# Kernel optimization log

Hardware: AMD Instinct MI355X
Metric: run time of the kernel (lower is better)

## Reference

```python
import jax, jax.numpy as jnp
import numpy as np

DIM, WIDTH = 5, 64
BATCH, N_SAVE = 4096, 64
RTOL, ATOL = 1e-3, 1e-6
SAFETY, FMIN, FMAX = 0.9, 0.2, 10.0
MAX_STEPS, DT0, EPS = 64, 0.1, 1e-6

# Tsit5 (Tsitouras 2011) Butcher tableau
A21 = 0.161
A31, A32 = -0.008480655492356989, 0.335480655492357
A41, A42, A43 = 2.8971530571054935, -6.359448489975075, 4.3622954328695815
A51, A52, A53, A54 = 5.325864828439257, -11.748883564062828, 7.4955393428898365, -0.09249506636175525
A61, A62, A63, A64, A65 = 5.86145544294642, -12.92096931784711, 8.159367898576159, -0.071584973281401, -0.028269050394068383
B1, B2, B3, B4, B5, B6 = 0.09646076681806523, 0.01, 0.4798896504144996, 1.379008574103742, -3.290069515436081, 2.324710524099774
# embedded 4th-order error coefficients (b - bhat)
E1, E2, E3, E4, E5, E6, E7 = (-0.00178001105222577714, -0.0008164344596567469,
    0.007880878010261995, -0.1447110071732629, 0.5823571654525552,
    -0.45808210592918697, 0.015151515151515152)


def _mlp(y, W1, b1, W2, b2, W3, b3, W4, b4):
    # eqx.nn.MLP(5, 5, width 64, depth 3, softplus)
    h = jax.nn.softplus(y @ W1.T + b1)
    h = jax.nn.softplus(h @ W2.T + b2)
    h = jax.nn.softplus(h @ W3.T + b3)
    return h @ W4.T + b4


def _solve_one(y0, t_eval, params):
    f = lambda y: _mlp(y, *params)
    t0, t1 = t_eval[0], t_eval[-1]
    # save points at/before t0 get y0
    ys0 = jnp.where((t_eval <= t0 + EPS)[:, None], y0[None, :], 0.0)

    def body(carry, _):
        t, y, h, ys = carry
        done = t >= t1 - EPS
        hc = jnp.where(done, 0.0, jnp.minimum(h, t1 - t))  # clip last step to t1
        k1 = f(y)
        k2 = f(y + hc * (A21 * k1))
        k3 = f(y + hc * (A31 * k1 + A32 * k2))
        k4 = f(y + hc * (A41 * k1 + A42 * k2 + A43 * k3))
        k5 = f(y + hc * (A51 * k1 + A52 * k2 + A53 * k3 + A54 * k4))
        k6 = f(y + hc * (A61 * k1 + A62 * k2 + A63 * k3 + A64 * k4 + A65 * k5))
        ynew = y + hc * (B1 * k1 + B2 * k2 + B3 * k3 + B4 * k4 + B5 * k5 + B6 * k6)
        k7 = f(ynew)  # FSAL stage, also used for error + interpolation
        err = hc * (E1 * k1 + E2 * k2 + E3 * k3 + E4 * k4 + E5 * k5 + E6 * k6 + E7 * k7)
        scale = ATOL + RTOL * jnp.maximum(jnp.abs(y), jnp.abs(ynew))
        enorm = jnp.sqrt(jnp.mean((err / scale) ** 2))
        enorm_c = jax.lax.stop_gradient(jnp.maximum(enorm, 1e-10))
        accept = enorm <= 1.0
        factor = jnp.clip(SAFETY * enorm_c ** -0.2, FMIN, FMAX)  # I-controller, order 5
        step_ok = accept & ~done
        t_next = jnp.where(step_ok, t + hc, t)
        y_next = jnp.where(step_ok, ynew, y)
        h_next = jnp.where(done, h, hc * factor)
        # cubic Hermite interpolation for save points inside (t, t_next]
        s = ((t_eval - t) / jnp.maximum(hc, 1e-12))[:, None]
        h00 = 2 * s**3 - 3 * s**2 + 1
        h10 = s**3 - 2 * s**2 + s
        h01 = -2 * s**3 + 3 * s**2
        h11 = s**3 - s**2
        yi = h00 * y + h10 * hc * k1 + h01 * ynew + h11 * hc * k7
        mask = (t_eval > t) & (t_eval <= t_next + EPS) & step_ok
        ys = jnp.where(mask[:, None], yi, ys)
        return (t_next, y_next, h_next, ys), None

    h0 = jnp.asarray(DT0, dtype=y0.dtype)
    (_, _, _, ys), _ = jax.lax.scan(body, (t0, y0, h0, ys0), None, length=MAX_STEPS)
    return ys  # [N_SAVE, DIM]


def setup_inputs() -> dict:
    key = jax.random.key(0)
    ks = jax.random.split(key, 9)
    y0 = jax.random.normal(ks[0], (BATCH, DIM), dtype=jnp.float32)
    t_eval = jnp.linspace(0.0, 1.0, N_SAVE, dtype=jnp.float32)

    def lin(k, out_d, in_d):
        lim = 1.0 / np.sqrt(in_d)
        kw, kb = jax.random.split(k)
        W = jax.random.uniform(kw, (out_d, in_d), jnp.float32, -lim, lim)
        b = jax.random.uniform(kb, (out_d,), jnp.float32, -lim, lim)
        return W, b

    W1, b1 = lin(ks[1], WIDTH, DIM)
    W2, b2 = lin(ks[2], WIDTH, WIDTH)
    W3, b3 = lin(ks[3], WIDTH, WIDTH)
    W4, b4 = lin(ks[4], DIM, WIDTH)
    return {"y0": y0, "t_eval": t_eval, "W1": W1, "b1": b1, "W2": W2, "b2": b2,
            "W3": W3, "b3": b3, "W4": W4, "b4": b4}


def reference(y0, t_eval, W1, b1, W2, b2, W3, b3, W4, b4):
    params = (W1, b1, W2, b2, W3, b3, W4, b4)
    return jax.vmap(lambda y: _solve_one(y, t_eval, params))(y0)  # [BATCH, N_SAVE, DIM]
```

## Files before the change

kernel.cpp:

```cpp
#include <hip/hip_runtime.h>
#include <cmath>

namespace {

constexpr int kDim = 5;
constexpr int kSave = 64;
constexpr int kTraj = 16;
constexpr int kThreads = 256;
constexpr int kMaxSteps = 64;
constexpr int HS = 72;
constexpr int SD = 8;

typedef _Float16 half8 __attribute__((ext_vector_type(8)));
typedef float f32x4 __attribute__((ext_vector_type(4)));

__device__ __forceinline__ float softplusf(float x) {
  return fmaxf(x, 0.0f) + __logf(1.0f + __expf(-fabsf(x)));
}

__global__ __launch_bounds__(kThreads, 1)
void node_tsit5_kernel(const float* __restrict__ gy0,
                       const float* __restrict__ gte,
                       const float* __restrict__ gW1, const float* __restrict__ gb1,
                       const float* __restrict__ gW2, const float* __restrict__ gb2,
                       const float* __restrict__ gW3, const float* __restrict__ gb3,
                       const float* __restrict__ gW4, const float* __restrict__ gb4,
                       float* __restrict__ out) {
  const float A21 = 0.161f;
  const float A31 = -0.008480655492356989f, A32 = 0.335480655492357f;
  const float A41 = 2.8971530571054935f, A42 = -6.359448489975075f, A43 = 4.3622954328695815f;
  const float A51 = 5.325864828439257f, A52 = -11.748883564062828f, A53 = 7.4955393428898365f,
              A54 = -0.09249506636175525f;
  const float A61 = 5.86145544294642f, A62 = -12.92096931784711f, A63 = 8.159367898576159f,
              A64 = -0.071584973281401f, A65 = -0.028269050394068383f;
  const float B1 = 0.09646076681806523f, B2 = 0.01f, B3 = 0.4798896504144996f,
              B4 = 1.379008574103742f, B5 = -3.290069515436081f, B6 = 2.324710524099774f;
  const float E1 = -0.00178001105222577714f, E2 = -0.0008164344596567469f,
              E3 = 0.007880878010261995f, E4 = -0.1447110071732629f, E5 = 0.5823571654525552f,
              E6 = -0.45808210592918697f, E7 = 0.015151515151515152f;

  __shared__ __align__(16) _Float16 h0[kTraj * HS], l0[kTraj * HS];
  __shared__ __align__(16) _Float16 h1[kTraj * HS], l1[kTraj * HS];
  __shared__ __align__(16) _Float16 h2[kTraj * HS], l2[kTraj * HS];
  __shared__ float sTe[kSave];
  __shared__ float sY[kTraj * SD], sYN[kTraj * SD], sK1[kTraj * SD], sK7[kTraj * SD];
  __shared__ float ctT[kTraj], ctH[kTraj], ctN[kTraj], ctO[kTraj];

  const int tid = threadIdx.x;
  const int bid = blockIdx.x;
  const int w = tid >> 6;
  const int ln = tid & 63;
  const int quad = ln >> 4;
  const int col = ln & 15;
  const int row0 = quad * 4;
  const int nn = (w << 4) | col;
  const bool cact = col < kDim;
  const bool w0 = (w == 0);

  half8 w2h[2], w3h[2], w4h[2], mfh[2];
  float w1r[kDim];
  #pragma unroll
  for (int d = 0; d < kDim; ++d) w1r[d] = gW1[nn * 5 + d];
  #pragma unroll
  for (int kf = 0; kf < 2; ++kf)
    #pragma unroll
    for (int j = 0; j < 8; ++j) {
      int kk2 = kf * 32 + quad * 8 + j;
      w2h[kf][j] = (_Float16)gW2[nn * 64 + kk2];
      w3h[kf][j] = (_Float16)gW3[nn * 64 + kk2];
      w4h[kf][j] = cact ? (_Float16)gW4[col * 64 + kk2] : (_Float16)0.0f;
      float m = 0.0f;
      #pragma unroll
      for (int d = 0; d < kDim; ++d) m = fmaf(w1r[d], gW4[d * 64 + kk2], m);
      mfh[kf][j] = (_Float16)m;
    }
  const float c1 = gb1[nn], c2 = gb2[nn], c3 = gb3[nn];
  const float c4 = cact ? gb4[col] : 0.0f;
  float cu = 0.0f;
  #pragma unroll
  for (int d = 0; d < kDim; ++d) cu = fmaf(w1r[d], gb4[d], cu);

  if (tid < kSave) sTe[tid] = gte[tid];
  if (tid < kTraj * kDim) {
    int t = tid & 15, d = tid >> 4;
    sY[t * SD + d] = gy0[(size_t)(bid * kTraj + t) * kDim + d];
  }
  {
    float* ob = out + (size_t)bid * kTraj * kSave * kDim;
    for (int idx = tid; idx < kTraj * kSave * kDim; idx += kThreads) ob[idx] = 0.0f;
  }

  f32x4 syr = {0, 0, 0, 0}, synr = {0, 0, 0, 0}, kk[7], uu[7], p_y;
  #pragma unroll
  for (int r = 0; r < 4; ++r) {
    const float* yr = gy0 + (size_t)(bid * kTraj + row0 + r) * kDim;
    float acc = c1;
    #pragma unroll
    for (int d = 0; d < kDim; ++d) acc = fmaf(w1r[d], yr[d], acc);
    p_y[r] = acc;
    if (cact) syr[r] = yr[col];
  }
  __syncthreads();

  const float t0v = sTe[0];
  const float t1v = sTe[kSave - 1];

  {
    int tt = tid & 15, gg = tid >> 4;
    float yv[kDim];
    #pragma unroll
    for (int d = 0; d < kDim; ++d) yv[d] = sY[tt * SD + d];
    #pragma unroll
    for (int q = 0; q < 4; ++q) {
      int n = 4 * gg + q;
      if (sTe[n] <= t0v + 1e-6f) {
        float* op = out + ((size_t)(bid * kTraj + tt) * kSave + n) * kDim;
        #pragma unroll
        for (int d = 0; d < kDim; ++d) op[d] = yv[d];
      }
    }
  }

  auto stageA = [&](f32x4 pre1) {
    #pragma unroll
    for (int r = 0; r < 4; ++r) {
      float s = softplusf(pre1[r]);
      _Float16 hi = (_Float16)s;
      h0[(row0 + r) * HS + nn] = hi;
      l0[(row0 + r) * HS + nn] = (_Float16)(s - (float)hi);
    }
  };

  auto evalR = [&](f32x4& kOut, f32x4& uOut) {
    {
      half8 ah0 = *(const half8*)(h0 + col * HS + quad * 8);
      half8 ah1 = *(const half8*)(h0 + col * HS + 32 + quad * 8);
      half8 al0 = *(const half8*)(l0 + col * HS + quad * 8);
      half8 al1 = *(const half8*)(l0 + col * HS + 32 + quad * 8);
      f32x4 a = {c2, c2, c2, c2};
      f32x4 b = {0, 0, 0, 0};
      a = __builtin_amdgcn_mfma_f32_16x16x32_f16(ah0, w2h[0], a, 0, 0, 0);
      b = __builtin_amdgcn_mfma_f32_16x16x32_f16(al0, w2h[0], b, 0, 0, 0);
      a = __builtin_amdgcn_mfma_f32_16x16x32_f16(ah1, w2h[1], a, 0, 0, 0);
      b = __builtin_amdgcn_mfma_f32_16x16x32_f16(al1, w2h[1], b, 0, 0, 0);
      a += b;
      #pragma unroll
      for (int r = 0; r < 4; ++r) {
        float s = softplusf(a[r]);
        _Float16 hi = (_Float16)s;
        h1[(row0 + r) * HS + nn] = hi;
        l1[(row0 + r) * HS + nn] = (_Float16)(s - (float)hi);
      }
    }
    __syncthreads();
    {
      half8 ah0 = *(const half8*)(h1 + col * HS + quad * 8);
      half8 ah1 = *(const half8*)(h1 + col * HS + 32 + quad * 8);
      half8 al0 = *(const half8*)(l1 + col * HS + quad * 8);
      half8 al1 = *(const half8*)(l1 + col * HS + 32 + quad * 8);
      f32x4 a = {c3, c3, c3, c3};
      f32x4 b = {0, 0, 0, 0};
      a = __builtin_amdgcn_mfma_f32_16x16x32_f16(ah0, w3h[0], a, 0, 0, 0);
      b = __builtin_amdgcn_mfma_f32_16x16x32_f16(al0, w3h[0], b, 0, 0, 0);
      a = __builtin_amdgcn_mfma_f32_16x16x32_f16(ah1, w3h[1], a, 0, 0, 0);
      b = __builtin_amdgcn_mfma_f32_16x16x32_f16(al1, w3h[1], b, 0, 0, 0);
      a += b;
      #pragma unroll
      for (int r = 0; r < 4; ++r) {
        float s = softplusf(a[r]);
        _Float16 hi = (_Float16)s;
        h2[(row0 + r) * HS + nn] = hi;
        l2[(row0 + r) * HS + nn] = (_Float16)(s - (float)hi);
      }
    }
    __syncthreads();
    {
      half8 ah0 = *(const half8*)(h2 + col * HS + quad * 8);
      half8 ah1 = *(const half8*)(h2 + col * HS + 32 + quad * 8);
      half8 al0 = *(const half8*)(l2 + col * HS + quad * 8);
      half8 al1 = *(const half8*)(l2 + col * HS + 32 + quad * 8);
      f32x4 ka = {c4, c4, c4, c4};
      f32x4 kb = {0, 0, 0, 0};
      f32x4 ua = {cu, cu, cu, cu};
      f32x4 ub = {0, 0, 0, 0};
      ka = __builtin_amdgcn_mfma_f32_16x16x32_f16(ah0, w4h[0], ka, 0, 0, 0);
      kb = __builtin_amdgcn_mfma_f32_16x16x32_f16(al0, w4h[0], kb, 0, 0, 0);
      ua = __builtin_amdgcn_mfma_f32_16x16x32_f16(ah0, mfh[0], ua, 0, 0, 0);
      ub = __builtin_amdgcn_mfma_f32_16x16x32_f16(al0, mfh[0], ub, 0, 0, 0);
      ka = __builtin_amdgcn_mfma_f32_16x16x32_f16(ah1, w4h[1], ka, 0, 0, 0);
      kb = __builtin_amdgcn_mfma_f32_16x16x32_f16(al1, w4h[1], kb, 0, 0, 0);
      ua = __builtin_amdgcn_mfma_f32_16x16x32_f16(ah1, mfh[1], ua, 0, 0, 0);
      ub = __builtin_amdgcn_mfma_f32_16x16x32_f16(al1, mfh[1], ub, 0, 0, 0);
      kOut = ka + kb;
      uOut = ua + ub;
    }
  };

  stageA(p_y);
  __syncthreads();
  evalR(kk[0], uu[0]);

  f32x4 tcur = {t0v, t0v, t0v, t0v};
  f32x4 hcur = {0.1f, 0.1f, 0.1f, 0.1f};
  f32x4 hcs, tOldr;
  bool dnr[4];
  bool alldone;

  auto head = [&]() {
    bool all4 = true;
    #pragma unroll
    for (int r = 0; r < 4; ++r) {
      bool d = tcur[r] >= t1v - 1e-6f;
      dnr[r] = d;
      all4 &= d;
      hcs[r] = d ? 0.0f : fminf(hcur[r], t1v - tcur[r]);
      tOldr[r] = tcur[r];
    }
    alldone = (__ballot(all4) == ~0ull);
  };

  head();
  if (!alldone) {
    f32x4 p1;
    #pragma unroll
    for (int r = 0; r < 4; ++r) p1[r] = fmaf(hcs[r], A21 * uu[0][r], p_y[r]);
    stageA(p1);
    __syncthreads();
  }

  for (int step = 0; step < kMaxSteps && !alldone; ++step) {
    f32x4 p1;
    evalR(kk[1], uu[1]);

    #pragma unroll
    for (int r = 0; r < 4; ++r)
      p1[r] = fmaf(hcs[r], fmaf(A32, uu[1][r], A31 * uu[0][r]), p_y[r]);
    stageA(p1); __syncthreads(); evalR(kk[2], uu[2]);

    #pragma unroll
    for (int r = 0; r < 4; ++r)
      p1[r] = fmaf(hcs[r], fmaf(A43, uu[2][r], fmaf(A42, uu[1][r], A41 * uu[0][r])), p_y[r]);
    stageA(p1); __syncthreads(); evalR(kk[3], uu[3]);

    #pragma unroll
    for (int r = 0; r < 4; ++r)
      p1[r] = fmaf(hcs[r], fmaf(A54, uu[3][r], fmaf(A53, uu[2][r],
                  fmaf(A52, uu[1][r], A51 * uu[0][r]))), p_y[r]);
    stageA(p1); __syncthreads(); evalR(kk[4], uu[4]);

    #pragma unroll
    for (int r = 0; r < 4; ++r)
      p1[r] = fmaf(hcs[r], fmaf(A65, uu[4][r], fmaf(A64, uu[3][r], fmaf(A63, uu[2][r],
                  fmaf(A62, uu[1][r], A61 * uu[0][r])))), p_y[r]);
    stageA(p1); __syncthreads(); evalR(kk[5], uu[5]);

    f32x4 bu;
    #pragma unroll
    for (int r = 0; r < 4; ++r) {
      bu[r] = fmaf(B6, uu[5][r], fmaf(B5, uu[4][r], fmaf(B4, uu[3][r],
              fmaf(B3, uu[2][r], fmaf(B2, uu[1][r], B1 * uu[0][r])))));
      synr[r] = fmaf(hcs[r], fmaf(B6, kk[5][r], fmaf(B5, kk[4][r], fmaf(B4, kk[3][r],
                 fmaf(B3, kk[2][r], fmaf(B2, kk[1][r], B1 * kk[0][r]))))), syr[r]);
      p1[r] = fmaf(hcs[r], bu[r], p_y[r]);
    }
    if (w0 && cact) {
      #pragma unroll
      for (int r = 0; r < 4; ++r) {
        int o = (row0 + r) * SD + col;
        sY[o] = syr[r];
        sYN[o] = synr[r];
        sK1[o] = kk[0][r];
      }
    }
    stageA(p1); __syncthreads(); evalR(kk[6], uu[6]);

    f32x4 rr2;
    #pragma unroll
    for (int r = 0; r < 4; ++r) {
      float err = hcs[r] * fmaf(E7, kk[6][r], fmaf(E6, kk[5][r], fmaf(E5, kk[4][r],
                  fmaf(E4, kk[3][r], fmaf(E3, kk[2][r], fmaf(E2, kk[1][r], E1 * kk[0][r]))))));
      float sc = fmaf(1e-3f, fmaxf(fabsf(syr[r]), fabsf(synr[r])), 1e-6f);
      float rr = err / sc;
      rr2[r] = cact ? rr * rr : 0.0f;
    }
    #pragma unroll
    for (int m = 1; m < 16; m <<= 1) {
      #pragma unroll
      for (int r = 0; r < 4; ++r) rr2[r] += __shfl_xor(rr2[r], m, 64);
    }

    bool okr[4];
    #pragma unroll
    for (int r = 0; r < 4; ++r) {
      float enorm = sqrtf(rr2[r] / 5.0f);
      float enc = fmaxf(enorm, 1e-10f);
      bool accept = enorm <= 1.0f;
      float factor = fminf(fmaxf(0.9f * __expf(-0.2f * __logf(enc)), 0.2f), 10.0f);
      bool ok = accept && !dnr[r];
      okr[r] = ok;
      tcur[r] = ok ? tcur[r] + hcs[r] : tcur[r];
      hcur[r] = dnr[r] ? hcur[r] : hcs[r] * factor;
    }

    if (w0 && cact) {
      #pragma unroll
      for (int r = 0; r < 4; ++r) sK7[(row0 + r) * SD + col] = kk[6][r];
    }
    if (w0 && col == 0) {
      #pragma unroll
      for (int r = 0; r < 4; ++r) {
        int m2 = row0 + r;
        ctT[m2] = tOldr[r];
        ctH[m2] = hcs[r];
        ctN[m2] = tcur[r];
        ctO[m2] = okr[r] ? 1.0f : 0.0f;
      }
    }

    #pragma unroll
    for (int r = 0; r < 4; ++r) {
      if (okr[r]) {
        syr[r] = synr[r];
        kk[0][r] = kk[6][r];
        uu[0][r] = uu[6][r];
        p_y[r] = fmaf(hcs[r], bu[r], p_y[r]);
      }
    }

    head();
    if (!alldone) {
      f32x4 pn;
      #pragma unroll
      for (int r = 0; r < 4; ++r) pn[r] = fmaf(hcs[r], A21 * uu[0][r], p_y[r]);
      stageA(pn);
    }
    __syncthreads();

    {
      int tt = tid & 15, gg = tid >> 4;
      if (ctO[tt] != 0.0f) {
        float tOld = ctT[tt], hcv = ctH[tt], tNew = ctN[tt];
        float inv = 1.0f / fmaxf(hcv, 1e-12f);
        float yv[kDim], ynv[kDim], k1v[kDim], k7v[kDim];
        #pragma unroll
        for (int d = 0; d < kDim; ++d) {
          yv[d] = sY[tt * SD + d];
          ynv[d] = sYN[tt * SD + d];
          k1v[d] = hcv * sK1[tt * SD + d];
          k7v[d] = hcv * sK7[tt * SD + d];
        }
        #pragma unroll
        for (int q = 0; q < 4; ++q) {
          int n = 4 * gg + q;
          float te = sTe[n];
          if (te > tOld && te <= tNew + 1e-6f) {
            float sx = (te - tOld) * inv;
            float s2 = sx * sx, s3 = s2 * sx;
            float h00 = 2.f * s3 - 3.f * s2 + 1.f;
            float h10 = s3 - 2.f * s2 + sx;
            float h01 = -2.f * s3 + 3.f * s2;
            float h11 = s3 - s2;
            float* op = out + ((size_t)(bid * kTraj + tt) * kSave + n) * kDim;
            #pragma unroll
            for (int d = 0; d < kDim; ++d)
              op[d] = h00 * yv[d] + h10 * k1v[d] + h01 * ynv[d] + h11 * k7v[d];
          }
        }
      }
    }
  }
}

}

extern "C" void kernel_launch(void* const* d_in, const int* in_sizes, int n_in,
                              void* d_out, int out_size, void* d_ws, size_t ws_size,
                              hipStream_t stream) {
  const float* y0 = (const float*)d_in[0];
  const float* te = (const float*)d_in[1];
  const float* W1 = (const float*)d_in[2];
  const float* b1 = (const float*)d_in[3];
  const float* W2 = (const float*)d_in[4];
  const float* b2 = (const float*)d_in[5];
  const float* W3 = (const float*)d_in[6];
  const float* b3 = (const float*)d_in[7];
  const float* W4 = (const float*)d_in[8];
  const float* b4 = (const float*)d_in[9];
  float* out = (float*)d_out;

  const int batch = in_sizes[0] / kDim;
  const int blocks = batch / kTraj;
  hipLaunchKernelGGL(node_tsit5_kernel, dim3(blocks), dim3(kThreads), 0, stream,
                     y0, te, W1, b1, W2, b2, W3, b3, W4, b4, out);
}
```

Measured before the change: 106.3 us.

## Stage outputs in shared memory, use lightweight barriers, prefetch A fragments

The output tile is buffered in LDS and written to global memory once, coalesced, at the end. This replaces the initial global zero fill and the scattered per-step interpolation stores. __syncthreads is swapped for an lgkmcnt-only wait plus s_barrier, so barriers no longer drain outstanding global stores. The first-layer A fragments for the next step are loaded right after the barrier, and the error-norm sqrt is folded into the log exponent. Risks include about 20 KB more LDS and barriers that no longer order global memory operations.

```diff
diff --git a/kernel.cpp b/kernel.cpp
--- a/kernel.cpp
+++ b/kernel.cpp
@@ -10,6 +10,7 @@
 constexpr int kMaxSteps = 64;
 constexpr int HS = 72;
 constexpr int SD = 8;
+constexpr int OS = kTraj * kDim;
 
 typedef _Float16 half8 __attribute__((ext_vector_type(8)));
 typedef float f32x4 __attribute__((ext_vector_type(4)));
@@ -17,6 +18,14 @@
 __device__ __forceinline__ float softplusf(float x) {
   return fmaxf(x, 0.0f) + __logf(1.0f + __expf(-fabsf(x)));
 }
+
+__device__ __forceinline__ void barrier_lgkm() {
+  asm volatile("s_waitcnt lgkmcnt(0)" ::: "memory");
+  __builtin_amdgcn_s_barrier();
+  asm volatile("" ::: "memory");
+}
+
+struct FragsA { half8 h0a, h1a, l0a, l1a; };
 
 __global__ __launch_bounds__(kThreads, 1)
 void node_tsit5_kernel(const float* __restrict__ gy0,
@@ -45,6 +54,7 @@
   __shared__ float sTe[kSave];
   __shared__ float sY[kTraj * SD], sYN[kTraj * SD], sK1[kTraj * SD], sK7[kTraj * SD];
   __shared__ float ctT[kTraj], ctH[kTraj], ctN[kTraj], ctO[kTraj];
+  __shared__ __align__(16) float sOut[kSave * OS];
 
   const int tid = threadIdx.x;
   const int bid = blockIdx.x;
@@ -86,8 +96,9 @@
     sY[t * SD + d] = gy0[(size_t)(bid * kTraj + t) * kDim + d];
   }
   {
-    float* ob = out + (size_t)bid * kTraj * kSave * kDim;
-    for (int idx = tid; idx < kTraj * kSave * kDim; idx += kThreads) ob[idx] = 0.0f;
+    f32x4 zz = {0.f, 0.f, 0.f, 0.f};
+    f32x4* z4 = (f32x4*)sOut;
+    for (int i = tid; i < (kSave * OS) / 4; i += kThreads) z4[i] = zz;
   }
 
   f32x4 syr = {0, 0, 0, 0}, synr = {0, 0, 0, 0}, kk[7], uu[7], p_y;
@@ -100,7 +111,7 @@
     p_y[r] = acc;
     if (cact) syr[r] = yr[col];
   }
-  __syncthreads();
+  barrier_lgkm();
 
   const float t0v = sTe[0];
   const float t1v = sTe[kSave - 1];
@@ -114,7 +125,7 @@
     for (int q = 0; q < 4; ++q) {
       int n = 4 * gg + q;
       if (sTe[n] <= t0v + 1e-6f) {
-        float* op = out + ((size_t)(bid * kTraj + tt) * kSave + n) * kDim;
+        float* op = sOut + n * OS + tt * kDim;
         #pragma unroll
         for (int d = 0; d < kDim; ++d) op[d] = yv[d];
       }
@@ -131,18 +142,23 @@
     }
   };
 
-  auto evalR = [&](f32x4& kOut, f32x4& uOut) {
+  auto loadA0 = [&]() {
+    FragsA f;
+    f.h0a = *(const half8*)(h0 + col * HS + quad * 8);
+    f.h1a = *(const half8*)(h0 + col * HS + 32 + quad * 8);
+    f.l0a = *(const half8*)(l0 + col * HS + quad * 8);
+    f.l1a = *(const half8*)(l0 + col * HS + 32 + quad * 8);
+    return f;
+  };
+
+  auto evalR = [&](FragsA f, f32x4& kOut, f32x4& uOut) {
     {
-      half8 ah0 = *(const half8*)(h0 + col * HS + quad * 8);
-      half8 ah1 = *(const half8*)(h0 + col * HS + 32 + quad * 8);
-      half8 al0 = *(const half8*)(l0 + col * HS + quad * 8);
-      half8 al1 = *(const half8*)(l0 + col * HS + 32 + quad * 8);
       f32x4 a = {c2, c2, c2, c2};
       f32x4 b = {0, 0, 0, 0};
-      a = __builtin_amdgcn_mfma_f32_16x16x32_f16(ah0, w2h[0], a, 0, 0, 0);
-      b = __builtin_amdgcn_mfma_f32_16x16x32_f16(al0, w2h[0], b, 0, 0, 0);
-      a = __builtin_amdgcn_mfma_f32_16x16x32_f16(ah1, w2h[1], a, 0, 0, 0);
-      b = __builtin_amdgcn_mfma_f32_16x16x32_f16(al1, w2h[1], b, 0, 0, 0);
+      a = __builtin_amdgcn_mfma_f32_16x16x32_f16(f.h0a, w2h[0], a, 0, 0, 0);
+      b = __builtin_amdgcn_mfma_f32_16x16x32_f16(f.l0a, w2h[0], b, 0, 0, 0);
+      a = __builtin_amdgcn_mfma_f32_16x16x32_f16(f.h1a, w2h[1], a, 0, 0, 0);
+      b = __builtin_amdgcn_mfma_f32_16x16x32_f16(f.l1a, w2h[1], b, 0, 0, 0);
       a += b;
       #pragma unroll
       for (int r = 0; r < 4; ++r) {
@@ -152,7 +168,7 @@
         l1[(row0 + r) * HS + nn] = (_Float16)(s - (float)hi);
       }
     }
-    __syncthreads();
+    barrier_lgkm();
     {
       half8 ah0 = *(const half8*)(h1 + col * HS + quad * 8);
       half8 ah1 = *(const half8*)(h1 + col * HS + 32 + quad * 8);
@@ -173,7 +189,7 @@
         l2[(row0 + r) * HS + nn] = (_Float16)(s - (float)hi);
       }
     }
-    __syncthreads();
+    barrier_lgkm();
     {
       half8 ah0 = *(const half8*)(h2 + col * HS + quad * 8);
       half8 ah1 = *(const half8*)(h2 + col * HS + 32 + quad * 8);
@@ -197,8 +213,8 @@
   };
 
   stageA(p_y);
-  __syncthreads();
-  evalR(kk[0], uu[0]);
+  barrier_lgkm();
+  evalR(loadA0(), kk[0], uu[0]);
 
   f32x4 tcur = {t0v, t0v, t0v, t0v};
   f32x4 hcur = {0.1f, 0.1f, 0.1f, 0.1f};
@@ -225,34 +241,35 @@
     #pragma unroll
     for (int r = 0; r < 4; ++r) p1[r] = fmaf(hcs[r], A21 * uu[0][r], p_y[r]);
     stageA(p1);
-    __syncthreads();
-  }
+  }
+  barrier_lgkm();
+  FragsA fNext = loadA0();
 
   for (int step = 0; step < kMaxSteps && !alldone; ++step) {
     f32x4 p1;
-    evalR(kk[1], uu[1]);
+    evalR(fNext, kk[1], uu[1]);
 
     #pragma unroll
     for (int r = 0; r < 4; ++r)
       p1[r] = fmaf(hcs[r], fmaf(A32, uu[1][r], A31 * uu[0][r]), p_y[r]);
-    stageA(p1); __syncthreads(); evalR(kk[2], uu[2]);
+    stageA(p1); barrier_lgkm(); evalR(loadA0(), kk[2], uu[2]);
 
     #pragma unroll
     for (int r = 0; r < 4; ++r)
       p1[r] = fmaf(hcs[r], fmaf(A43, uu[2][r], fmaf(A42, uu[1][r], A41 * uu[0][r])), p_y[r]);
-    stageA(p1); __syncthreads(); evalR(kk[3], uu[3]);
+    stageA(p1); barrier_lgkm(); evalR(loadA0(), kk[3], uu[3]);
 
     #pragma unroll
     for (int r = 0; r < 4; ++r)
       p1[r] = fmaf(hcs[r], fmaf(A54, uu[3][r], fmaf(A53, uu[2][r],
                   fmaf(A52, uu[1][r], A51 * uu[0][r]))), p_y[r]);
-    stageA(p1); __syncthreads(); evalR(kk[4], uu[4]);
+    stageA(p1); barrier_lgkm(); evalR(loadA0(), kk[4], uu[4]);
 
     #pragma unroll
     for (int r = 0; r < 4; ++r)
       p1[r] = fmaf(hcs[r], fmaf(A65, uu[4][r], fmaf(A64, uu[3][r], fmaf(A63, uu[2][r],
                   fmaf(A62, uu[1][r], A61 * uu[0][r])))), p_y[r]);
-    stageA(p1); __syncthreads(); evalR(kk[5], uu[5]);
+    stageA(p1); barrier_lgkm(); evalR(loadA0(), kk[5], uu[5]);
 
     f32x4 bu;
     #pragma unroll
@@ -272,7 +289,7 @@
         sK1[o] = kk[0][r];
       }
     }
-    stageA(p1); __syncthreads(); evalR(kk[6], uu[6]);
+    stageA(p1); barrier_lgkm(); evalR(loadA0(), kk[6], uu[6]);
 
     f32x4 rr2;
     #pragma unroll
@@ -292,10 +309,10 @@
     bool okr[4];
     #pragma unroll
     for (int r = 0; r < 4; ++r) {
-      float enorm = sqrtf(rr2[r] / 5.0f);
-      float enc = fmaxf(enorm, 1e-10f);
-      bool accept = enorm <= 1.0f;
-      float factor = fminf(fmaxf(0.9f * __expf(-0.2f * __logf(enc)), 0.2f), 10.0f);
+      float e2 = rr2[r] * 0.2f;
+      bool accept = e2 <= 1.0f;
+      float e2c = fmaxf(e2, 1e-20f);
+      float factor = fminf(fmaxf(0.9f * __expf(-0.1f * __logf(e2c)), 0.2f), 10.0f);
       bool ok = accept && !dnr[r];
       okr[r] = ok;
       tcur[r] = ok ? tcur[r] + hcs[r] : tcur[r];
@@ -334,7 +351,10 @@
       for (int r = 0; r < 4; ++r) pn[r] = fmaf(hcs[r], A21 * uu[0][r], p_y[r]);
       stageA(pn);
     }
-    __syncthreads();
+    __attribute__((unused)) int dummy = 0;
+    barrier_lgkm();
+
+    fNext = loadA0();
 
     {
       int tt = tid & 15, gg = tid >> 4;
@@ -360,13 +380,25 @@
             float h10 = s3 - 2.f * s2 + sx;
             float h01 = -2.f * s3 + 3.f * s2;
             float h11 = s3 - s2;
-            float* op = out + ((size_t)(bid * kTraj + tt) * kSave + n) * kDim;
+            float* op = sOut + n * OS + tt * kDim;
             #pragma unroll
             for (int d = 0; d < kDim; ++d)
               op[d] = h00 * yv[d] + h10 * k1v[d] + h01 * ynv[d] + h11 * k7v[d];
           }
         }
       }
+    }
+  }
+
+  barrier_lgkm();
+  {
+    float* ob = out + (size_t)bid * (kTraj * kSave * kDim);
+    for (int idx = tid; idx < kTraj * kSave * kDim; idx += kThreads) {
+      int traj = idx / (kSave * kDim);
+      int p = idx - traj * (kSave * kDim);
+      int n = p / kDim;
+      int d = p - n * kDim;
+      ob[idx] = sOut[n * OS + traj * kDim + d];
     }
   }
 }
```

New measurement: 106.3 us. About the same (+0.0%).
